# Kernel optimization log

Hardware: AMD Instinct MI355X
Metric: run time of the kernel (lower is better)

Reference implementation:

```python
import jax, jax.numpy as jnp
import numpy as np

B, S, V, E, H = 1024, 256, 32000, 300, 256  # batch, enc_len, vocab, embed_dim, hidden_dim
ENC = 3 * H  # encoder feature width (768)


def setup_inputs() -> dict:
    key = jax.random.key(0)
    ks = jax.random.split(key, 14)
    s = 0.02
    return {
        "x": jax.random.randint(ks[0], (B,), 0, V),
        "h": jax.random.normal(ks[1], (B, H), jnp.float32),
        "c": jax.random.normal(ks[2], (B, H), jnp.float32),
        "encoder_outputs": jax.random.normal(ks[3], (B, S, ENC), jnp.float32),
        "emb": jax.random.normal(ks[4], (V, E), jnp.float32) * s,
        "attn_w": jax.random.normal(ks[5], (H, 4 * H), jnp.float32) * s,
        "attn_b": jnp.zeros((H,), jnp.float32),
        "v_w": jax.random.normal(ks[6], (H,), jnp.float32) * s,
        "w_ih": jax.random.normal(ks[7], (4 * H, E + ENC), jnp.float32) * s,
        "w_hh": jax.random.normal(ks[8], (4 * H, H), jnp.float32) * s,
        "b_ih": jnp.zeros((4 * H,), jnp.float32),
        "b_hh": jnp.zeros((4 * H,), jnp.float32),
        "out_w": jax.random.normal(ks[9], (V, H), jnp.float32) * s,
        "out_b": jnp.zeros((V,), jnp.float32),
    }


def reference(x, h, c, encoder_outputs, emb, attn_w, attn_b, v_w,
              w_ih, w_hh, b_ih, b_hh, out_w, out_b):
    # embedding (dropout is identity in eval mode)
    e = emb[x]  # [B, E]
    # additive attention: tanh(W [h; enc] + b); split W to avoid materializing the concat
    w_h, w_e = attn_w[:, :H], attn_w[:, H:]
    energy = jnp.tanh(h @ w_h.T[:, :] [None].squeeze(0) @ jnp.eye(H, dtype=h.dtype) if False else
                      (h @ w_h.T)[:, None, :] + jnp.einsum('bsd,hd->bsh', encoder_outputs, w_e) + attn_b)  # [B,S,H]
    scores = jnp.einsum('bsh,h->bs', energy, v_w)
    attn = jax.nn.softmax(scores, axis=1)  # [B,S]
    context = jnp.einsum('bs,bsd->bd', attn, encoder_outputs)  # [B, 3H]
    # single-step LSTM (PyTorch gate order: i, f, g, o)
    xi = jnp.concatenate([e, context], axis=-1)  # [B, E+3H]
    gates = xi @ w_ih.T + b_ih + h @ w_hh.T + b_hh  # [B, 4H]
    i, f, g, o = jnp.split(gates, 4, axis=-1)
    c2 = jax.nn.sigmoid(f) * c + jax.nn.sigmoid(i) * jnp.tanh(g)
    h2 = jax.nn.sigmoid(o) * jnp.tanh(c2)
    logits = h2 @ out_w.T + out_b  # [B, V]
    return logits, h2, c2
```

## Files before the change

kernel.cpp:

```cpp
#include <hip/hip_runtime.h>
#include <hip/hip_bf16.h>
#include <stdint.h>

#define BDIM 1024
#define SDIM 256
#define VDIM 32000
#define EDIM 300
#define HDIM 256
#define ENCD 768
#define G4H  1024
#define KXI  1344

typedef short bf16x8 __attribute__((ext_vector_type(8)));
typedef float f32x4  __attribute__((ext_vector_type(4)));

static __device__ __forceinline__ unsigned short f2bf(float f) {
  __hip_bfloat16 b = __float2bfloat16(f);
  return *reinterpret_cast<unsigned short*>(&b);
}
static __device__ __forceinline__ unsigned pk2(float x, float y) {
  float2 f; f.x = x; f.y = y;
  __hip_bfloat162 h = __float22bfloat162_rn(f);
  return *reinterpret_cast<unsigned*>(&h);
}
static __device__ __forceinline__ float bf2f(unsigned short u) {
  union { unsigned u; float f; } v; v.u = ((unsigned)u) << 16; return v.f;
}
static __device__ __forceinline__ float sigf(float x) {
  return 1.0f / (1.0f + __expf(-x));
}
static __device__ __forceinline__ float tanh_fast(float x) {
  return 1.0f - 2.0f / (__expf(2.0f * x) + 1.0f);
}
static __device__ __forceinline__ int swz_off(int row, int kbyte) {
  return row * 1536 + (kbyte ^ ((row & 7) << 4));
}

__global__ void k_prep(const float* __restrict__ attn_w, const float* __restrict__ w_ih,
                       const float* __restrict__ w_hh, const float* __restrict__ out_w,
                       unsigned short* __restrict__ w_e_frag, float* __restrict__ w_hT,
                       unsigned short* __restrict__ Wb, unsigned short* __restrict__ outw_b) {
  const long NWE = (long)HDIM * ENCD;
  const long NWH = (long)HDIM * HDIM;
  const long NWB = (long)G4H * KXI;
  const long NOW = (long)VDIM * HDIM;
  const long total = NWE + NWH + NWB + NOW;
  for (long idx = blockIdx.x * 256L + threadIdx.x; idx < total; idx += gridDim.x * 256L) {
    long i = idx;
    if (i < NWE) {
      int e    = (int)(i & 7);
      int f    = (int)(i >> 3);
      int lane = f & 63;
      int n    = (f >> 6) & 1;
      int r2   = f >> 7;
      int kt   = r2 % 24;
      int w    = r2 / 24;
      int j    = 32 * w + 16 * n + (lane & 15);
      int k    = 32 * kt + (lane >> 4) * 8 + e;
      w_e_frag[i] = f2bf(attn_w[j * (4 * HDIM) + HDIM + k]);
    } else if ((i -= NWE) < NWH) {
      int k = (int)(i / HDIM), j = (int)(i % HDIM);
      w_hT[i] = attn_w[j * (4 * HDIM) + k];
    } else if ((i -= NWH) < NWB) {
      int g = (int)(i / KXI), k = (int)(i % KXI);
      float v = 0.f;
      if (k < EDIM + ENCD) v = w_ih[(long)g * (EDIM + ENCD) + k];
      else if (k < EDIM + ENCD + HDIM) v = w_hh[(long)g * HDIM + (k - (EDIM + ENCD))];
      Wb[i] = f2bf(v);
    } else {
      i -= NWB;
      outw_b[i] = f2bf(out_w[i]);
    }
  }
}

__global__ void k_hwb(const float* __restrict__ h, const float* __restrict__ w_hT,
                      const float* __restrict__ attn_b, float* __restrict__ hwb) {
  int b = blockIdx.x, t = threadIdx.x;
  __shared__ float hl[HDIM];
  hl[t] = h[b * HDIM + t];
  __syncthreads();
  float acc = attn_b[t];
#pragma unroll 8
  for (int k = 0; k < HDIM; ++k) acc += hl[k] * w_hT[k * HDIM + t];
  hwb[b * HDIM + t] = acc;
}

__launch_bounds__(512, 4)
__global__ void k_energy_ctx(const float* __restrict__ enc, const unsigned short* __restrict__ w_e_frag,
                             const float* __restrict__ hwb, const float* __restrict__ v_w,
                             float* __restrict__ ctx_part, float* __restrict__ denom_part) {
  const int b = blockIdx.x >> 3;
  const int st = blockIdx.x & 7;
  const int s0 = st * 32;
  const int t = threadIdx.x;
  const int lane = t & 63;
  const int w = t >> 6;
  const int li = lane & 15;
  const int lg = lane >> 4;

  __shared__ __align__(16) unsigned short encT[32 * ENCD];
  __shared__ float scores_lds[8 * 32];
  __shared__ float p_lds[32];

  const float* encB = enc + (long)(b * SDIM + s0) * ENCD;
  const int jw = 32 * w;
  const unsigned short* fragW = w_e_frag + (((long)w * 24 * 2) * 64 + lane) * 8;

  float4 sv[12];
#pragma unroll
  for (int u = 0; u < 12; ++u)
    sv[u] = *(const float4*)(encB + 4 * t + 2048 * u);

  bf16x8 bfr[4][2];
#pragma unroll
  for (int p = 0; p < 4; ++p)
#pragma unroll
    for (int n = 0; n < 2; ++n)
      bfr[p][n] = *(const bf16x8*)(fragW + ((p * 2 + n) * 64) * 8);

  float hw0 = hwb[b * HDIM + jw + li];
  float hw1 = hwb[b * HDIM + jw + 16 + li];
  float vw0 = v_w[jw + li];
  float vw1 = v_w[jw + 16 + li];

#pragma unroll
  for (int u = 0; u < 12; ++u) {
    const int flat = 4 * t + 2048 * u;
    const int row = flat / ENCD;
    const int col = flat - row * ENCD;
    uint2 pk;
    pk.x = pk2(sv[u].x, sv[u].y);
    pk.y = pk2(sv[u].z, sv[u].w);
    *(uint2*)((char*)encT + swz_off(row, col * 2)) = pk;
  }

  f32x4 acc[2][2];
#pragma unroll
  for (int m = 0; m < 2; m++)
#pragma unroll
    for (int n = 0; n < 2; n++) { f32x4 z = {0.f, 0.f, 0.f, 0.f}; acc[m][n] = z; }

  __syncthreads();

  bf16x8 afr[2][2];
#pragma unroll
  for (int p = 0; p < 2; ++p)
#pragma unroll
    for (int m = 0; m < 2; ++m)
      afr[p][m] = *(const bf16x8*)((const char*)encT + swz_off(16 * m + li, (p * 32 + lg * 8) * 2));

#pragma unroll
  for (int kt = 0; kt < 24; ++kt) {
    const int kb = kt & 3, ka = kt & 1;
#pragma unroll
    for (int m = 0; m < 2; m++)
#pragma unroll
      for (int n = 0; n < 2; n++)
        acc[m][n] = __builtin_amdgcn_mfma_f32_16x16x32_bf16(afr[ka][m], bfr[kb][n], acc[m][n], 0, 0, 0);
    if (kt + 4 < 24) {
#pragma unroll
      for (int n = 0; n < 2; ++n)
        bfr[kb][n] = *(const bf16x8*)(fragW + (((kt + 4) * 2 + n) * 64) * 8);
    }
    if (kt + 2 < 24) {
      const int kn2 = (kt + 2) * 32;
#pragma unroll
      for (int m = 0; m < 2; ++m)
        afr[ka][m] = *(const bf16x8*)((const char*)encT + swz_off(16 * m + li, (kn2 + lg * 8) * 2));
    }
  }

  float val[2][4];
#pragma unroll
  for (int m = 0; m < 2; m++)
#pragma unroll
    for (int r = 0; r < 4; r++) {
      float v0 = tanh_fast(acc[m][0][r] + hw0) * vw0 + tanh_fast(acc[m][1][r] + hw1) * vw1;
      v0 += __shfl_xor(v0, 1);
      v0 += __shfl_xor(v0, 2);
      v0 += __shfl_xor(v0, 4);
      v0 += __shfl_xor(v0, 8);
      val[m][r] = v0;
    }
  if (li < 4) {
    scores_lds[w * 32 + 4 * lg + li]      = val[0][li];
    scores_lds[w * 32 + 16 + 4 * lg + li] = val[1][li];
  }
  __syncthreads();
  if (t < 32) {
    float sc = 0.f;
#pragma unroll
    for (int ww = 0; ww < 8; ++ww) sc += scores_lds[ww * 32 + t];
    float p = __expf(sc);
    p_lds[t] = p;
    float dsum = p;
    dsum += __shfl_xor(dsum, 1);
    dsum += __shfl_xor(dsum, 2);
    dsum += __shfl_xor(dsum, 4);
    dsum += __shfl_xor(dsum, 8);
    dsum += __shfl_xor(dsum, 16);
    if (t == 0) denom_part[b * 8 + st] = dsum;
  }
  __syncthreads();
  if (t < 384) {
    float cx = 0.f, cy = 0.f;
#pragma unroll
    for (int s = 0; s < 32; ++s) {
      float p = p_lds[s];
      unsigned u = *(const unsigned*)((const char*)encT + swz_off(s, 4 * t));
      cx += p * bf2f((unsigned short)(u & 0xffffu));
      cy += p * bf2f((unsigned short)(u >> 16));
    }
    float* cp = ctx_part + (long)(b * 8 + st) * ENCD + 2 * t;
    cp[0] = cx; cp[1] = cy;
  }
}

__global__ void k_xi(const int* __restrict__ x, const float* __restrict__ emb,
                     const float* __restrict__ h, const float* __restrict__ ctx_part,
                     const float* __restrict__ denom_part, unsigned short* __restrict__ xi_b) {
  int b = blockIdx.x, t = threadIdx.x;
  float denom = 0.f;
#pragma unroll
  for (int st = 0; st < 8; ++st) denom += denom_part[b * 8 + st];
  float inv = 1.0f / denom;
#pragma unroll
  for (int u = 0; u < 3; ++u) {
    int d = t + 256 * u;
    float s = 0.f;
#pragma unroll
    for (int st = 0; st < 8; ++st) s += ctx_part[(long)(b * 8 + st) * ENCD + d];
    xi_b[(long)b * KXI + EDIM + d] = f2bf(s * inv);
  }
  int xv = x[b];
  for (int cc = t; cc < EDIM; cc += 256)
    xi_b[(long)b * KXI + cc] = f2bf(emb[(long)xv * EDIM + cc]);
  xi_b[(long)b * KXI + EDIM + ENCD + t] = f2bf(h[b * HDIM + t]);
  if (t < KXI - (EDIM + ENCD + HDIM))
    xi_b[(long)b * KXI + (EDIM + ENCD + HDIM) + t] = 0;
}

__launch_bounds__(256)
__global__ void k_gemm_bt(const unsigned short* __restrict__ A, const unsigned short* __restrict__ Bt,
                          const float* __restrict__ bias1, const float* __restrict__ bias2,
                          float* __restrict__ out, int N, int K, int MTILES) {
  int bx = blockIdx.x;
  int mt = bx % MTILES, nt = bx / MTILES;
  int row0 = mt * 128, col0 = nt * 128;
  int t = threadIdx.x, lane = t & 63, w = t >> 6;
  int li = lane & 15, lg = lane >> 4;
  int wr = (w >> 1) * 64, wc = (w & 1) * 64;
  __shared__ __align__(16) unsigned short As[2][128 * 32];
  __shared__ __align__(16) unsigned short Bs[2][128 * 32];
  f32x4 acc[4][4];
#pragma unroll
  for (int m = 0; m < 4; m++)
#pragma unroll
    for (int n = 0; n < 4; n++) { f32x4 z = {0.f, 0.f, 0.f, 0.f}; acc[m][n] = z; }

  auto stage = [&](int buf, int k0) {
#pragma unroll
    for (int rep = 0; rep < 2; ++rep) {
      int slot = t + rep * 256;
      int r = slot >> 2, sg = slot & 3;
      uint4 va = *(const uint4*)(A + (long)(row0 + r) * K + k0 + sg * 8);
      uint4 vb = *(const uint4*)(Bt + (long)(col0 + r) * K + k0 + sg * 8);
      *(uint4*)&As[buf][r * 32 + sg * 8] = va;
      *(uint4*)&Bs[buf][r * 32 + sg * 8] = vb;
    }
  };

  stage(0, 0);
  __syncthreads();
  const int nk = K / 32;
  for (int kt = 0; kt < nk; ++kt) {
    if (kt + 1 < nk) stage((kt + 1) & 1, (kt + 1) * 32);
    int cb = kt & 1;
    bf16x8 a[4], bb[4];
#pragma unroll
    for (int m = 0; m < 4; m++) a[m] = *(const bf16x8*)&As[cb][(wr + 16 * m + li) * 32 + lg * 8];
#pragma unroll
    for (int n = 0; n < 4; n++) bb[n] = *(const bf16x8*)&Bs[cb][(wc + 16 * n + li) * 32 + lg * 8];
#pragma unroll
    for (int m = 0; m < 4; m++)
#pragma unroll
      for (int n = 0; n < 4; n++)
        acc[m][n] = __builtin_amdgcn_mfma_f32_16x16x32_bf16(a[m], bb[n], acc[m][n], 0, 0, 0);
    __syncthreads();
  }

#pragma unroll
  for (int n = 0; n < 4; n++) {
    int col = col0 + wc + 16 * n + li;
    float bs = bias1[col];
    if (bias2) bs += bias2[col];
#pragma unroll
    for (int m = 0; m < 4; m++) {
      int rb = row0 + wr + 16 * m + lg * 4;
#pragma unroll
      for (int r = 0; r < 4; r++)
        out[(long)(rb + r) * N + col] = acc[m][n][r] + bs;
    }
  }
}

__global__ void k_lstm(const float* __restrict__ gates, const float* __restrict__ c,
                       float* __restrict__ h2, float* __restrict__ c2,
                       unsigned short* __restrict__ h2b) {
  int b = blockIdx.x, j = threadIdx.x;
  const float* g = gates + (long)b * G4H;
  float ig = sigf(g[j]);
  float fg = sigf(g[HDIM + j]);
  float gg = tanh_fast(g[2 * HDIM + j]);
  float og = sigf(g[3 * HDIM + j]);
  float cv = c[b * HDIM + j];
  float c2v = fg * cv + ig * gg;
  float h2v = og * tanh_fast(c2v);
  c2[b * HDIM + j] = c2v;
  h2[b * HDIM + j] = h2v;
  h2b[b * HDIM + j] = f2bf(h2v);
}

extern "C" void kernel_launch(void* const* d_in, const int* in_sizes, int n_in,
                              void* d_out, int out_size, void* d_ws, size_t ws_size,
                              hipStream_t stream) {
  const int*   x      = (const int*)d_in[0];
  const float* h      = (const float*)d_in[1];
  const float* c      = (const float*)d_in[2];
  const float* enc    = (const float*)d_in[3];
  const float* emb    = (const float*)d_in[4];
  const float* attn_w = (const float*)d_in[5];
  const float* attn_b = (const float*)d_in[6];
  const float* v_w    = (const float*)d_in[7];
  const float* w_ih   = (const float*)d_in[8];
  const float* w_hh   = (const float*)d_in[9];
  const float* b_ih   = (const float*)d_in[10];
  const float* b_hh   = (const float*)d_in[11];
  const float* out_w  = (const float*)d_in[12];
  const float* out_b  = (const float*)d_in[13];
  float* out = (float*)d_out;

  char* ws = (char*)d_ws;
  float* hwb             = (float*)(ws + 0);
  unsigned short* w_e_fr = (unsigned short*)(ws + 1048576);
  float* w_hT            = (float*)(ws + 1441792);
  float* ctx_part        = (float*)(ws + 1703936);
  float* denom_part      = (float*)(ws + 26869760);
  unsigned short* Wb     = (unsigned short*)(ws + 26902528);
  unsigned short* xi_b   = (unsigned short*)(ws + 29655040);
  float* gates           = (float*)(ws + 32407552);
  unsigned short* h2b    = (unsigned short*)(ws + 36601856);
  unsigned short* outw_b = (unsigned short*)(ws + 37126144);
  if (ws_size < 53510144u) return;

  k_prep<<<2048, 256, 0, stream>>>(attn_w, w_ih, w_hh, out_w, w_e_fr, w_hT, Wb, outw_b);
  k_hwb<<<1024, 256, 0, stream>>>(h, w_hT, attn_b, hwb);
  k_energy_ctx<<<8192, 512, 0, stream>>>(enc, w_e_fr, hwb, v_w, ctx_part, denom_part);
  k_xi<<<1024, 256, 0, stream>>>(x, emb, h, ctx_part, denom_part, xi_b);
  k_gemm_bt<<<64, 256, 0, stream>>>(xi_b, Wb, b_ih, b_hh, gates, G4H, KXI, 8);
  k_lstm<<<1024, 256, 0, stream>>>(gates, c, out + (long)BDIM * VDIM,
                                   out + (long)BDIM * VDIM + (long)BDIM * HDIM, h2b);
  k_gemm_bt<<<2000, 256, 0, stream>>>(h2b, outw_b, out_b, nullptr, out, VDIM, HDIM, 8);
}
```

Baseline: 395.0 us.

## Make energy-context kernel persistent with double-buffered encoder tiles and register-resident weights

```diff
diff --git a/kernel.cpp b/kernel.cpp
--- a/kernel.cpp
+++ b/kernel.cpp
@@ -86,134 +86,159 @@
   hwb[b * HDIM + t] = acc;
 }
 
-__launch_bounds__(512, 4)
+__launch_bounds__(512, 2)
 __global__ void k_energy_ctx(const float* __restrict__ enc, const unsigned short* __restrict__ w_e_frag,
                              const float* __restrict__ hwb, const float* __restrict__ v_w,
                              float* __restrict__ ctx_part, float* __restrict__ denom_part) {
-  const int b = blockIdx.x >> 3;
-  const int st = blockIdx.x & 7;
-  const int s0 = st * 32;
   const int t = threadIdx.x;
   const int lane = t & 63;
   const int w = t >> 6;
   const int li = lane & 15;
   const int lg = lane >> 4;
-
-  __shared__ __align__(16) unsigned short encT[32 * ENCD];
+  const int jw = 32 * w;
+
+  __shared__ __align__(16) unsigned short encT[2][32 * ENCD];
   __shared__ float scores_lds[8 * 32];
   __shared__ float p_lds[32];
 
-  const float* encB = enc + (long)(b * SDIM + s0) * ENCD;
-  const int jw = 32 * w;
-  const unsigned short* fragW = w_e_frag + (((long)w * 24 * 2) * 64 + lane) * 8;
-
-  float4 sv[12];
-#pragma unroll
-  for (int u = 0; u < 12; ++u)
-    sv[u] = *(const float4*)(encB + 4 * t + 2048 * u);
-
-  bf16x8 bfr[4][2];
-#pragma unroll
-  for (int p = 0; p < 4; ++p)
+  const int NT = 16;
+  const int tile0 = blockIdx.x * NT;
+
+  const unsigned short* fragW = w_e_frag + (((long)w * 48) * 64 + lane) * 8;
+  bf16x8 bfr[24][2];
+#pragma unroll
+  for (int kt = 0; kt < 24; ++kt)
 #pragma unroll
     for (int n = 0; n < 2; ++n)
-      bfr[p][n] = *(const bf16x8*)(fragW + ((p * 2 + n) * 64) * 8);
-
-  float hw0 = hwb[b * HDIM + jw + li];
-  float hw1 = hwb[b * HDIM + jw + 16 + li];
-  float vw0 = v_w[jw + li];
-  float vw1 = v_w[jw + 16 + li];
-
-#pragma unroll
-  for (int u = 0; u < 12; ++u) {
-    const int flat = 4 * t + 2048 * u;
-    const int row = flat / ENCD;
-    const int col = flat - row * ENCD;
-    uint2 pk;
-    pk.x = pk2(sv[u].x, sv[u].y);
-    pk.y = pk2(sv[u].z, sv[u].w);
-    *(uint2*)((char*)encT + swz_off(row, col * 2)) = pk;
-  }
-
-  f32x4 acc[2][2];
-#pragma unroll
-  for (int m = 0; m < 2; m++)
-#pragma unroll
-    for (int n = 0; n < 2; n++) { f32x4 z = {0.f, 0.f, 0.f, 0.f}; acc[m][n] = z; }
-
+      bfr[kt][n] = *(const bf16x8*)(fragW + ((kt * 2 + n) * 64) * 8);
+
+  const float vw0 = v_w[jw + li];
+  const float vw1 = v_w[jw + 16 + li];
+
+  {
+    const float* encB = enc + (long)tile0 * 32 * ENCD;
+    float4 sv[12];
+#pragma unroll
+    for (int u = 0; u < 12; ++u)
+      sv[u] = *(const float4*)(encB + 4 * t + 2048 * u);
+#pragma unroll
+    for (int u = 0; u < 12; ++u) {
+      const int flat = 4 * t + 2048 * u;
+      const int row = flat / ENCD;
+      const int col = flat - row * ENCD;
+      uint2 pk;
+      pk.x = pk2(sv[u].x, sv[u].y);
+      pk.y = pk2(sv[u].z, sv[u].w);
+      *(uint2*)((char*)&encT[0][0] + swz_off(row, col * 2)) = pk;
+    }
+  }
   __syncthreads();
 
-  bf16x8 afr[2][2];
-#pragma unroll
-  for (int p = 0; p < 2; ++p)
-#pragma unroll
-    for (int m = 0; m < 2; ++m)
-      afr[p][m] = *(const bf16x8*)((const char*)encT + swz_off(16 * m + li, (p * 32 + lg * 8) * 2));
-
-#pragma unroll
-  for (int kt = 0; kt < 24; ++kt) {
-    const int kb = kt & 3, ka = kt & 1;
+  for (int it = 0; it < NT; ++it) {
+    const int tile = tile0 + it;
+    const int b = tile >> 3, st = tile & 7;
+    const char* cbuf = (const char*)&encT[it & 1][0];
+    char* nbuf = (char*)&encT[(it + 1) & 1][0];
+
+    float4 sv[12];
+    const bool more = (it + 1 < NT);
+    if (more) {
+      const float* encN = enc + (long)(tile + 1) * 32 * ENCD;
+#pragma unroll
+      for (int u = 0; u < 12; ++u)
+        sv[u] = *(const float4*)(encN + 4 * t + 2048 * u);
+    }
+
+    const float hw0 = hwb[b * HDIM + jw + li];
+    const float hw1 = hwb[b * HDIM + jw + 16 + li];
+
+    f32x4 acc[2][2];
 #pragma unroll
     for (int m = 0; m < 2; m++)
 #pragma unroll
-      for (int n = 0; n < 2; n++)
-        acc[m][n] = __builtin_amdgcn_mfma_f32_16x16x32_bf16(afr[ka][m], bfr[kb][n], acc[m][n], 0, 0, 0);
-    if (kt + 4 < 24) {
-#pragma unroll
-      for (int n = 0; n < 2; ++n)
-        bfr[kb][n] = *(const bf16x8*)(fragW + (((kt + 4) * 2 + n) * 64) * 8);
-    }
-    if (kt + 2 < 24) {
-      const int kn2 = (kt + 2) * 32;
+      for (int n = 0; n < 2; n++) { f32x4 z = {0.f, 0.f, 0.f, 0.f}; acc[m][n] = z; }
+
+    bf16x8 afr[2][2];
+#pragma unroll
+    for (int p = 0; p < 2; ++p)
 #pragma unroll
       for (int m = 0; m < 2; ++m)
-        afr[ka][m] = *(const bf16x8*)((const char*)encT + swz_off(16 * m + li, (kn2 + lg * 8) * 2));
-    }
-  }
-
-  float val[2][4];
-#pragma unroll
-  for (int m = 0; m < 2; m++)
-#pragma unroll
-    for (int r = 0; r < 4; r++) {
-      float v0 = tanh_fast(acc[m][0][r] + hw0) * vw0 + tanh_fast(acc[m][1][r] + hw1) * vw1;
-      v0 += __shfl_xor(v0, 1);
-      v0 += __shfl_xor(v0, 2);
-      v0 += __shfl_xor(v0, 4);
-      v0 += __shfl_xor(v0, 8);
-      val[m][r] = v0;
-    }
-  if (li < 4) {
-    scores_lds[w * 32 + 4 * lg + li]      = val[0][li];
-    scores_lds[w * 32 + 16 + 4 * lg + li] = val[1][li];
-  }
-  __syncthreads();
-  if (t < 32) {
-    float sc = 0.f;
-#pragma unroll
-    for (int ww = 0; ww < 8; ++ww) sc += scores_lds[ww * 32 + t];
-    float p = __expf(sc);
-    p_lds[t] = p;
-    float dsum = p;
-    dsum += __shfl_xor(dsum, 1);
-    dsum += __shfl_xor(dsum, 2);
-    dsum += __shfl_xor(dsum, 4);
-    dsum += __shfl_xor(dsum, 8);
-    dsum += __shfl_xor(dsum, 16);
-    if (t == 0) denom_part[b * 8 + st] = dsum;
-  }
-  __syncthreads();
-  if (t < 384) {
-    float cx = 0.f, cy = 0.f;
-#pragma unroll
-    for (int s = 0; s < 32; ++s) {
-      float p = p_lds[s];
-      unsigned u = *(const unsigned*)((const char*)encT + swz_off(s, 4 * t));
-      cx += p * bf2f((unsigned short)(u & 0xffffu));
-      cy += p * bf2f((unsigned short)(u >> 16));
-    }
-    float* cp = ctx_part + (long)(b * 8 + st) * ENCD + 2 * t;
-    cp[0] = cx; cp[1] = cy;
+        afr[p][m] = *(const bf16x8*)(cbuf + swz_off(16 * m + li, (p * 32 + lg * 8) * 2));
+#pragma unroll
+    for (int kt = 0; kt < 24; ++kt) {
+      const int ka = kt & 1;
+#pragma unroll
+      for (int m = 0; m < 2; m++)
+#pragma unroll
+        for (int n = 0; n < 2; n++)
+          acc[m][n] = __builtin_amdgcn_mfma_f32_16x16x32_bf16(afr[ka][m], bfr[kt][n], acc[m][n], 0, 0, 0);
+      if (kt + 2 < 24) {
+        const int kn2 = (kt + 2) * 32;
+#pragma unroll
+        for (int m = 0; m < 2; ++m)
+          afr[ka][m] = *(const bf16x8*)(cbuf + swz_off(16 * m + li, (kn2 + lg * 8) * 2));
+      }
+    }
+
+    if (more) {
+#pragma unroll
+      for (int u = 0; u < 12; ++u) {
+        const int flat = 4 * t + 2048 * u;
+        const int row = flat / ENCD;
+        const int col = flat - row * ENCD;
+        uint2 pk;
+        pk.x = pk2(sv[u].x, sv[u].y);
+        pk.y = pk2(sv[u].z, sv[u].w);
+        *(uint2*)(nbuf + swz_off(row, col * 2)) = pk;
+      }
+    }
+
+    float val[2][4];
+#pragma unroll
+    for (int m = 0; m < 2; m++)
+#pragma unroll
+      for (int r = 0; r < 4; r++) {
+        float v0 = tanh_fast(acc[m][0][r] + hw0) * vw0 + tanh_fast(acc[m][1][r] + hw1) * vw1;
+        v0 += __shfl_xor(v0, 1);
+        v0 += __shfl_xor(v0, 2);
+        v0 += __shfl_xor(v0, 4);
+        v0 += __shfl_xor(v0, 8);
+        val[m][r] = v0;
+      }
+    if (li < 4) {
+      scores_lds[w * 32 + 4 * lg + li]      = val[0][li];
+      scores_lds[w * 32 + 16 + 4 * lg + li] = val[1][li];
+    }
+    __syncthreads();
+    if (t < 32) {
+      float sc = 0.f;
+#pragma unroll
+      for (int ww = 0; ww < 8; ++ww) sc += scores_lds[ww * 32 + t];
+      float p = __expf(sc);
+      p_lds[t] = p;
+      float dsum = p;
+      dsum += __shfl_xor(dsum, 1);
+      dsum += __shfl_xor(dsum, 2);
+      dsum += __shfl_xor(dsum, 4);
+      dsum += __shfl_xor(dsum, 8);
+      dsum += __shfl_xor(dsum, 16);
+      if (t == 0) denom_part[b * 8 + st] = dsum;
+    }
+    __syncthreads();
+
+    if (t < 384) {
+      float cx = 0.f, cy = 0.f;
+#pragma unroll
+      for (int s = 0; s < 32; ++s) {
+        float p = p_lds[s];
+        unsigned u = *(const unsigned*)(cbuf + swz_off(s, 4 * t));
+        cx += p * bf2f((unsigned short)(u & 0xffffu));
+        cy += p * bf2f((unsigned short)(u >> 16));
+      }
+      float* cp = ctx_part + (long)(b * 8 + st) * ENCD + 2 * t;
+      cp[0] = cx; cp[1] = cy;
+    }
+    __syncthreads();
   }
 }
 
@@ -356,7 +381,7 @@
 
   k_prep<<<2048, 256, 0, stream>>>(attn_w, w_ih, w_hh, out_w, w_e_fr, w_hT, Wb, outw_b);
   k_hwb<<<1024, 256, 0, stream>>>(h, w_hT, attn_b, hwb);
-  k_energy_ctx<<<8192, 512, 0, stream>>>(enc, w_e_fr, hwb, v_w, ctx_part, denom_part);
+  k_energy_ctx<<<512, 512, 0, stream>>>(enc, w_e_fr, hwb, v_w, ctx_part, denom_part);
   k_xi<<<1024, 256, 0, stream>>>(x, emb, h, ctx_part, denom_part, xi_b);
   k_gemm_bt<<<64, 256, 0, stream>>>(xi_b, Wb, b_ih, b_hh, gates, G4H, KXI, 8);
   k_lstm<<<1024, 256, 0, stream>>>(gates, c, out + (long)BDIM * VDIM,
```

Measured after the change: 827.6 us. 2.09x slower.
